# Optimization experiments

Measured on AMD Instinct MI355X. Metric: run time of the kernel, lower is better.

## Reference

```python
import jax, jax.numpy as jnp
import numpy as np

B, N, DIN = 16, 1024, 256
HEADS, OUT_DIM = 4, 256
F = OUT_DIM // HEADS  # per-head feature dim
NEG_SLOPE = 0.2
MASK_VAL = -1e9


def setup_inputs() -> dict:
    key = jax.random.key(0)
    k1, k2, k3, k4, k5, k6 = jax.random.split(key, 6)
    x = jax.random.normal(k1, (B, N, DIN), dtype=jnp.float32)
    adj = jax.random.uniform(k2, (B, N, N), dtype=jnp.float32)  # >0.5 -> edge
    # GATConv learned params (Glorot-ish scale)
    W = jax.random.normal(k3, (DIN, HEADS, F), dtype=jnp.float32) * (1.0 / np.sqrt(DIN))
    a_src = jax.random.normal(k4, (HEADS, F), dtype=jnp.float32) * (1.0 / np.sqrt(F))
    a_dst = jax.random.normal(k5, (HEADS, F), dtype=jnp.float32) * (1.0 / np.sqrt(F))
    bias = jax.random.normal(k6, (OUT_DIM,), dtype=jnp.float32) * 0.01
    return {"x": x, "adj": adj, "W": W, "a_src": a_src, "a_dst": a_dst, "bias": bias}


def reference(x, adj, W, a_src, a_dst, bias):
    # GAT over a dense adjacency mask: mathematically identical to
    # per-sample tf.where edge extraction + edge-list GATConv (softmax over
    # j with adj[b,i,j] > 0.5), but fully vectorized over the batch.
    b, n, _ = x.shape
    h = jnp.einsum('bnd,dhf->bnhf', x, W)                  # [B,N,H,F]
    e_src = jnp.einsum('bnhf,hf->bhn', h, a_src)           # source logits
    e_dst = jnp.einsum('bnhf,hf->bhn', h, a_dst)           # target logits
    # e[b,h,i,j]: edge j -> i
    e = e_dst[:, :, :, None] + e_src[:, :, None, :]        # [B,H,N,N]
    e = jax.nn.leaky_relu(e, NEG_SLOPE)
    mask = (adj > 0.5)[:, None, :, :]                      # [B,1,N,N]
    e = jnp.where(mask, e, MASK_VAL)
    attn = jax.nn.softmax(e, axis=-1)                      # softmax over sources j
    out = jnp.einsum('bhij,bjhf->bihf', attn, h)           # aggregate messages
    out = out.reshape(b, n, HEADS * F) + bias              # concat heads + bias
    return out
```

## Files before the change

### kernel.cpp

```cpp
#include <hip/hip_runtime.h>

#define B_    16
#define N_    1024
#define DIN_  256
#define H_    4
#define F_    64
#define COUT_ 256
#define NEG_  0.2f
#define LOG2E_ 1.4426950408889634f

typedef __bf16 bf16x8 __attribute__((ext_vector_type(8)));
typedef float  f32x4  __attribute__((ext_vector_type(4)));
typedef unsigned short u16x8 __attribute__((ext_vector_type(8)));
typedef unsigned short u16x4 __attribute__((ext_vector_type(4)));
typedef unsigned int   u32x4 __attribute__((ext_vector_type(4)));

__device__ __forceinline__ unsigned short f2bf(float f) {
    unsigned u = __builtin_bit_cast(unsigned, f);
    u += 0x7fffu + ((u >> 16) & 1u);
    return (unsigned short)(u >> 16);
}

__global__ __launch_bounds__(256) void prep_kernel(
    const float* __restrict__ W, unsigned short* __restrict__ Wtp) {
    const int c = blockIdx.x, k = threadIdx.x;
    const int w = c >> 6, ft = (c >> 4) & 3, l15 = c & 15;
    const int it = k >> 5, q = (k >> 3) & 3, jj = k & 7;
    const int ln = q * 16 + l15;
    Wtp[((((w * 8 + it) * 4 + ft) * 64) + ln) * 8 + jj] = f2bf(W[k * COUT_ + c]);
}

__global__ __launch_bounds__(256, 4) void stage_kernel(
    const float* __restrict__ adj, const float* __restrict__ x,
    const unsigned short* __restrict__ Wtp, const float* __restrict__ a_src,
    const float* __restrict__ a_dst, unsigned int* __restrict__ mask,
    unsigned short* __restrict__ hp, float* __restrict__ e_src,
    float* __restrict__ e_dst) {
    __shared__ unsigned short xs[16][264];
    const int w  = threadIdx.x >> 6;
    const int ln = threadIdx.x & 63;

    if (blockIdx.x < 4096) {
        const int row = blockIdx.x * 4 + w;
        const int b = row >> 10, i = row & (N_ - 1);
        const float* ar = adj + (size_t)row * N_ + ln * 4;
#pragma unroll
        for (int c = 0; c < 4; c++) {
            f32x4 v = *(const f32x4*)(ar + c * 256);
            unsigned nib = 0;
#pragma unroll
            for (int e = 0; e < 4; e++)
                nib |= (v[e] > 0.5f) ? (1u << e) : 0u;
            unsigned word = nib << ((ln & 7) * 4);
            word |= __shfl_xor(word, 1);
            word |= __shfl_xor(word, 2);
            word |= __shfl_xor(word, 4);
            if ((ln & 7) == 0) {
                const int jc = c * 8 + (ln >> 3);
                mask[(b * 32 + jc) * N_ + i] = word;
            }
        }
    } else {
        const int blk = blockIdx.x - 4096;
        const int b   = blk & 15;
        const int it0 = (blk >> 4) * 16;
        const int l15 = ln & 15;
        const int q   = ln >> 4;

#pragma unroll
        for (int s = 0; s < 4; s++) {
            const int row = w * 4 + s;
            f32x4 xv = *(const f32x4*)(x + (size_t)(b * N_ + it0 + row) * DIN_ + ln * 4);
            unsigned lo = (unsigned)f2bf(xv[0]) | ((unsigned)f2bf(xv[1]) << 16);
            unsigned hi = (unsigned)f2bf(xv[2]) | ((unsigned)f2bf(xv[3]) << 16);
            unsigned long long hb = (unsigned long long)lo | ((unsigned long long)hi << 32);
            *(unsigned long long*)&xs[row][ln * 4] = hb;
        }
        __syncthreads();

        f32x4 acc[4];
#pragma unroll
        for (int ft = 0; ft < 4; ft++) acc[ft] = (f32x4)0.0f;

        const unsigned short* wb = Wtp + (w * 8) * 4 * 64 * 8 + ln * 8;
#pragma unroll
        for (int it = 0; it < 8; it++) {
            bf16x8 af = *(const bf16x8*)&xs[l15][it * 32 + q * 8];
#pragma unroll
            for (int ft = 0; ft < 4; ft++) {
                bf16x8 bf = *((const bf16x8*)(wb + (it * 4 + ft) * 512));
                acc[ft] = __builtin_amdgcn_mfma_f32_16x16x32_bf16(af, bf, acc[ft], 0, 0, 0);
            }
        }

        const int jg = it0 >> 5;
        const int q2 = 2 * ((it0 >> 4) & 1) + (q >> 1);
#pragma unroll
        for (int ft = 0; ft < 4; ft++) {
            u16x4 hb;
#pragma unroll
            for (int r = 0; r < 4; r++) hb[r] = f2bf(acc[ft][r]);
            const size_t addr =
                (size_t)((((b * H_ + w) * 32 + jg) * 4 + ft) * 64 + q2 * 16 + l15) * 8 + (q & 1) * 4;
            *((u16x4*)(hp + addr)) = hb;
        }

        float as_v[4], ad_v[4];
#pragma unroll
        for (int ft = 0; ft < 4; ft++) {
            as_v[ft] = a_src[w * F_ + ft * 16 + l15];
            ad_v[ft] = a_dst[w * F_ + ft * 16 + l15];
        }
        float ps[4], pd[4];
#pragma unroll
        for (int r = 0; r < 4; r++) {
            ps[r] = 0.0f; pd[r] = 0.0f;
#pragma unroll
            for (int ft = 0; ft < 4; ft++) {
                ps[r] += acc[ft][r] * as_v[ft];
                pd[r] += acc[ft][r] * ad_v[ft];
            }
        }
#pragma unroll
        for (int off = 1; off <= 8; off <<= 1)
#pragma unroll
            for (int r = 0; r < 4; r++) {
                ps[r] += __shfl_xor(ps[r], off);
                pd[r] += __shfl_xor(pd[r], off);
            }
        float vs = (l15 == 0) ? ps[0] : (l15 == 1) ? ps[1] : (l15 == 2) ? ps[2] : ps[3];
        float vd = (l15 == 0) ? pd[0] : (l15 == 1) ? pd[1] : (l15 == 2) ? pd[2] : pd[3];
        if (l15 < 4) {
            const int i = it0 + q * 4 + l15;
            e_src[(b * H_ + w) * N_ + i] = vs * LOG2E_;
            e_dst[(b * H_ + w) * N_ + i] = vd * LOG2E_;
        }
    }
}

__global__ __launch_bounds__(512, 4) void gat_attn_kernel(
    const unsigned int* __restrict__ mask, const unsigned short* __restrict__ hp,
    const float* __restrict__ e_src, const float* __restrict__ e_dst,
    const float* __restrict__ bias, float* __restrict__ out) {
    const int lid = ((blockIdx.x & 7) << 6) | (blockIdx.x >> 3);
    const int b   = lid >> 5;
    const int it0 = (lid & 31) * 32;
    const int w8  = threadIdx.x >> 6;
    const int h   = w8 & 3;
    const int jh  = w8 >> 2;
    const int ln  = threadIdx.x & 63;
    const int l15 = ln & 15;
    const int q   = ln >> 4;

    __shared__ float lds[H_][2][5][64][4];

    float edv[2];
    edv[0] = e_dst[(b * H_ + h) * N_ + it0 + l15];
    edv[1] = e_dst[(b * H_ + h) * N_ + it0 + 16 + l15];

    const float* es_base          = e_src + (b * H_ + h) * N_;
    const unsigned short* hp_base = hp + (size_t)((b * H_ + h) * 32) * 2048 + ln * 8;
    const unsigned int* mk0       = mask + b * 32 * N_ + it0;

    f32x4 acc[2][4];
    f32x4 accs[2];
#pragma unroll
    for (int mt = 0; mt < 2; mt++) {
#pragma unroll
        for (int ft = 0; ft < 4; ft++) acc[mt][ft] = (f32x4)0.0f;
        accs[mt] = (f32x4)0.0f;
    }

    u16x8 ones_u;
#pragma unroll
    for (int jj = 0; jj < 8; jj++) ones_u[jj] = 0x3F80;
    const bf16x8 ones = __builtin_bit_cast(bf16x8, ones_u);

    for (int jg = jh * 16; jg < jh * 16 + 16; jg++) {
        const unsigned short* hf = hp_base + jg * 2048;
        bf16x8 bfr0 = *((const bf16x8*)(hf + 0 * 512));
        bf16x8 bfr1 = *((const bf16x8*)(hf + 1 * 512));
        bf16x8 bfr2 = *((const bf16x8*)(hf + 2 * 512));
        bf16x8 bfr3 = *((const bf16x8*)(hf + 3 * 512));
        f32x4 e0 = *(const f32x4*)(es_base + jg * 32 + q * 8);
        f32x4 e1 = *(const f32x4*)(es_base + jg * 32 + q * 8 + 4);
        const unsigned m0 = mk0[jg * N_ + l15];
        const unsigned m1 = mk0[jg * N_ + 16 + l15];

        float es8[8] = {e0[0], e0[1], e0[2], e0[3], e1[0], e1[1], e1[2], e1[3]};

        bf16x8 afr[2];
#pragma unroll
        for (int mt = 0; mt < 2; mt++) {
            const unsigned mq = ((mt ? m1 : m0) >> (q * 8)) & 0xffu;
            u32x4 up;
#pragma unroll
            for (int p2 = 0; p2 < 4; p2++) {
                float t0 = edv[mt] + es8[2 * p2];
                float t1 = edv[mt] + es8[2 * p2 + 1];
                t0 = fmaxf(t0, NEG_ * t0);
                t1 = fmaxf(t1, NEG_ * t1);
                float p0 = __builtin_amdgcn_exp2f(t0);
                float p1 = __builtin_amdgcn_exp2f(t1);
                p0 = ((mq >> (2 * p2)) & 1u) ? p0 : 0.0f;
                p1 = ((mq >> (2 * p2 + 1)) & 1u) ? p1 : 0.0f;
                up[p2] = __builtin_amdgcn_perm(__builtin_bit_cast(unsigned, p1),
                                               __builtin_bit_cast(unsigned, p0),
                                               0x07060302u);
            }
            afr[mt] = __builtin_bit_cast(bf16x8, up);
        }
#pragma unroll
        for (int mt = 0; mt < 2; mt++) {
            acc[mt][0] = __builtin_amdgcn_mfma_f32_16x16x32_bf16(afr[mt], bfr0, acc[mt][0], 0, 0, 0);
            acc[mt][1] = __builtin_amdgcn_mfma_f32_16x16x32_bf16(afr[mt], bfr1, acc[mt][1], 0, 0, 0);
            acc[mt][2] = __builtin_amdgcn_mfma_f32_16x16x32_bf16(afr[mt], bfr2, acc[mt][2], 0, 0, 0);
            acc[mt][3] = __builtin_amdgcn_mfma_f32_16x16x32_bf16(afr[mt], bfr3, acc[mt][3], 0, 0, 0);
            accs[mt]   = __builtin_amdgcn_mfma_f32_16x16x32_bf16(afr[mt], ones, accs[mt], 0, 0, 0);
        }
    }

    if (jh == 1) {
#pragma unroll
        for (int mt = 0; mt < 2; mt++) {
#pragma unroll
            for (int ft = 0; ft < 4; ft++)
                *(f32x4*)&lds[h][mt][ft][ln][0] = acc[mt][ft];
            *(f32x4*)&lds[h][mt][4][ln][0] = accs[mt];
        }
    }
    __syncthreads();
    if (jh == 0) {
#pragma unroll
        for (int mt = 0; mt < 2; mt++) {
#pragma unroll
            for (int ft = 0; ft < 4; ft++)
                acc[mt][ft] += *(const f32x4*)&lds[h][mt][ft][ln][0];
            accs[mt] += *(const f32x4*)&lds[h][mt][4][ln][0];
        }
        float bias_v[4];
#pragma unroll
        for (int ft = 0; ft < 4; ft++) bias_v[ft] = bias[h * F_ + ft * 16 + l15];
#pragma unroll
        for (int mt = 0; mt < 2; mt++) {
            f32x4 rinv;
#pragma unroll
            for (int r = 0; r < 4; r++) rinv[r] = 1.0f / accs[mt][r];
#pragma unroll
            for (int ft = 0; ft < 4; ft++)
#pragma unroll
                for (int r = 0; r < 4; r++) {
                    const int i = it0 + mt * 16 + q * 4 + r;
                    const int c = h * F_ + ft * 16 + l15;
                    out[(size_t)(b * N_ + i) * COUT_ + c] = acc[mt][ft][r] * rinv[r] + bias_v[ft];
                }
        }
    }
}

extern "C" void kernel_launch(void* const* d_in, const int* in_sizes, int n_in,
                              void* d_out, int out_size, void* d_ws, size_t ws_size,
                              hipStream_t stream) {
    const float* x     = (const float*)d_in[0];
    const float* adj   = (const float*)d_in[1];
    const float* W     = (const float*)d_in[2];
    const float* a_src = (const float*)d_in[3];
    const float* a_dst = (const float*)d_in[4];
    const float* bias  = (const float*)d_in[5];
    float* out = (float*)d_out;

    char* ws = (char*)d_ws;
    unsigned short* Wtp = (unsigned short*)ws;
    unsigned short* hp  = (unsigned short*)(ws + 131072);
    float* e_src        = (float*)(ws + 131072 + 8388608);
    float* e_dst        = (float*)(ws + 131072 + 8388608 + 262144);
    unsigned int* mask  = (unsigned int*)(ws + 131072 + 8388608 + 524288);

    prep_kernel<<<256, 256, 0, stream>>>(W, Wtp);
    stage_kernel<<<5120, 256, 0, stream>>>(adj, x, Wtp, a_src, a_dst, mask, hp, e_src, e_dst);
    gat_attn_kernel<<<512, 512, 0, stream>>>(mask, hp, e_src, e_dst, bias, out);
}
```

Baseline: 150.0 us.

## Read adjacency directly in attention kernel instead of precomputing bitmask

Drops the bit-packed mask pass from the staging kernel and has the attention kernel load the fp32 adjacency rows and threshold them inline. This avoids writing and rereading a mask buffer and shrinks the staging launch. The cost is that the attention kernel's inner loop now streams the full 64 MB adjacency, 32 bytes per row per lane, which adds memory traffic and latency on the main compute kernel's critical path.

Measured after the change: 162.6 us. 1.08x slower.

```diff
diff --git a/kernel.cpp b/kernel.cpp
--- a/kernel.cpp
+++ b/kernel.cpp
@@ -31,115 +31,92 @@
 }
 
 __global__ __launch_bounds__(256, 4) void stage_kernel(
-    const float* __restrict__ adj, const float* __restrict__ x,
-    const unsigned short* __restrict__ Wtp, const float* __restrict__ a_src,
-    const float* __restrict__ a_dst, unsigned int* __restrict__ mask,
+    const float* __restrict__ x, const unsigned short* __restrict__ Wtp,
+    const float* __restrict__ a_src, const float* __restrict__ a_dst,
     unsigned short* __restrict__ hp, float* __restrict__ e_src,
     float* __restrict__ e_dst) {
     __shared__ unsigned short xs[16][264];
     const int w  = threadIdx.x >> 6;
     const int ln = threadIdx.x & 63;
 
-    if (blockIdx.x < 4096) {
-        const int row = blockIdx.x * 4 + w;
-        const int b = row >> 10, i = row & (N_ - 1);
-        const float* ar = adj + (size_t)row * N_ + ln * 4;
-#pragma unroll
-        for (int c = 0; c < 4; c++) {
-            f32x4 v = *(const f32x4*)(ar + c * 256);
-            unsigned nib = 0;
-#pragma unroll
-            for (int e = 0; e < 4; e++)
-                nib |= (v[e] > 0.5f) ? (1u << e) : 0u;
-            unsigned word = nib << ((ln & 7) * 4);
-            word |= __shfl_xor(word, 1);
-            word |= __shfl_xor(word, 2);
-            word |= __shfl_xor(word, 4);
-            if ((ln & 7) == 0) {
-                const int jc = c * 8 + (ln >> 3);
-                mask[(b * 32 + jc) * N_ + i] = word;
-            }
-        }
-    } else {
-        const int blk = blockIdx.x - 4096;
-        const int b   = blk & 15;
-        const int it0 = (blk >> 4) * 16;
-        const int l15 = ln & 15;
-        const int q   = ln >> 4;
-
-#pragma unroll
-        for (int s = 0; s < 4; s++) {
-            const int row = w * 4 + s;
-            f32x4 xv = *(const f32x4*)(x + (size_t)(b * N_ + it0 + row) * DIN_ + ln * 4);
-            unsigned lo = (unsigned)f2bf(xv[0]) | ((unsigned)f2bf(xv[1]) << 16);
-            unsigned hi = (unsigned)f2bf(xv[2]) | ((unsigned)f2bf(xv[3]) << 16);
-            unsigned long long hb = (unsigned long long)lo | ((unsigned long long)hi << 32);
-            *(unsigned long long*)&xs[row][ln * 4] = hb;
-        }
-        __syncthreads();
-
-        f32x4 acc[4];
-#pragma unroll
-        for (int ft = 0; ft < 4; ft++) acc[ft] = (f32x4)0.0f;
-
-        const unsigned short* wb = Wtp + (w * 8) * 4 * 64 * 8 + ln * 8;
-#pragma unroll
-        for (int it = 0; it < 8; it++) {
-            bf16x8 af = *(const bf16x8*)&xs[l15][it * 32 + q * 8];
-#pragma unroll
-            for (int ft = 0; ft < 4; ft++) {
-                bf16x8 bf = *((const bf16x8*)(wb + (it * 4 + ft) * 512));
-                acc[ft] = __builtin_amdgcn_mfma_f32_16x16x32_bf16(af, bf, acc[ft], 0, 0, 0);
-            }
-        }
-
-        const int jg = it0 >> 5;
-        const int q2 = 2 * ((it0 >> 4) & 1) + (q >> 1);
+    const int blk = blockIdx.x;
+    const int b   = blk & 15;
+    const int it0 = (blk >> 4) * 16;
+    const int l15 = ln & 15;
+    const int q   = ln >> 4;
+
+#pragma unroll
+    for (int s = 0; s < 4; s++) {
+        const int row = w * 4 + s;
+        f32x4 xv = *(const f32x4*)(x + (size_t)(b * N_ + it0 + row) * DIN_ + ln * 4);
+        unsigned lo = (unsigned)f2bf(xv[0]) | ((unsigned)f2bf(xv[1]) << 16);
+        unsigned hi = (unsigned)f2bf(xv[2]) | ((unsigned)f2bf(xv[3]) << 16);
+        unsigned long long hb = (unsigned long long)lo | ((unsigned long long)hi << 32);
+        *(unsigned long long*)&xs[row][ln * 4] = hb;
+    }
+    __syncthreads();
+
+    f32x4 acc[4];
+#pragma unroll
+    for (int ft = 0; ft < 4; ft++) acc[ft] = (f32x4)0.0f;
+
+    const unsigned short* wb = Wtp + (w * 8) * 4 * 64 * 8 + ln * 8;
+#pragma unroll
+    for (int it = 0; it < 8; it++) {
+        bf16x8 af = *(const bf16x8*)&xs[l15][it * 32 + q * 8];
 #pragma unroll
         for (int ft = 0; ft < 4; ft++) {
-            u16x4 hb;
-#pragma unroll
-            for (int r = 0; r < 4; r++) hb[r] = f2bf(acc[ft][r]);
-            const size_t addr =
-                (size_t)((((b * H_ + w) * 32 + jg) * 4 + ft) * 64 + q2 * 16 + l15) * 8 + (q & 1) * 4;
-            *((u16x4*)(hp + addr)) = hb;
-        }
-
-        float as_v[4], ad_v[4];
+            bf16x8 bf = *((const bf16x8*)(wb + (it * 4 + ft) * 512));
+            acc[ft] = __builtin_amdgcn_mfma_f32_16x16x32_bf16(af, bf, acc[ft], 0, 0, 0);
+        }
+    }
+
+    const int jg = it0 >> 5;
+    const int q2 = 2 * ((it0 >> 4) & 1) + (q >> 1);
+#pragma unroll
+    for (int ft = 0; ft < 4; ft++) {
+        u16x4 hb;
+#pragma unroll
+        for (int r = 0; r < 4; r++) hb[r] = f2bf(acc[ft][r]);
+        const size_t addr =
+            (size_t)((((b * H_ + w) * 32 + jg) * 4 + ft) * 64 + q2 * 16 + l15) * 8 + (q & 1) * 4;
+        *((u16x4*)(hp + addr)) = hb;
+    }
+
+    float as_v[4], ad_v[4];
+#pragma unroll
+    for (int ft = 0; ft < 4; ft++) {
+        as_v[ft] = a_src[w * F_ + ft * 16 + l15];
+        ad_v[ft] = a_dst[w * F_ + ft * 16 + l15];
+    }
+    float ps[4], pd[4];
+#pragma unroll
+    for (int r = 0; r < 4; r++) {
+        ps[r] = 0.0f; pd[r] = 0.0f;
 #pragma unroll
         for (int ft = 0; ft < 4; ft++) {
-            as_v[ft] = a_src[w * F_ + ft * 16 + l15];
-            ad_v[ft] = a_dst[w * F_ + ft * 16 + l15];
-        }
-        float ps[4], pd[4];
+            ps[r] += acc[ft][r] * as_v[ft];
+            pd[r] += acc[ft][r] * ad_v[ft];
+        }
+    }
+#pragma unroll
+    for (int off = 1; off <= 8; off <<= 1)
 #pragma unroll
         for (int r = 0; r < 4; r++) {
-            ps[r] = 0.0f; pd[r] = 0.0f;
-#pragma unroll
-            for (int ft = 0; ft < 4; ft++) {
-                ps[r] += acc[ft][r] * as_v[ft];
-                pd[r] += acc[ft][r] * ad_v[ft];
-            }
-        }
-#pragma unroll
-        for (int off = 1; off <= 8; off <<= 1)
-#pragma unroll
-            for (int r = 0; r < 4; r++) {
-                ps[r] += __shfl_xor(ps[r], off);
-                pd[r] += __shfl_xor(pd[r], off);
-            }
-        float vs = (l15 == 0) ? ps[0] : (l15 == 1) ? ps[1] : (l15 == 2) ? ps[2] : ps[3];
-        float vd = (l15 == 0) ? pd[0] : (l15 == 1) ? pd[1] : (l15 == 2) ? pd[2] : pd[3];
-        if (l15 < 4) {
-            const int i = it0 + q * 4 + l15;
-            e_src[(b * H_ + w) * N_ + i] = vs * LOG2E_;
-            e_dst[(b * H_ + w) * N_ + i] = vd * LOG2E_;
-        }
+            ps[r] += __shfl_xor(ps[r], off);
+            pd[r] += __shfl_xor(pd[r], off);
+        }
+    float vs = (l15 == 0) ? ps[0] : (l15 == 1) ? ps[1] : (l15 == 2) ? ps[2] : ps[3];
+    float vd = (l15 == 0) ? pd[0] : (l15 == 1) ? pd[1] : (l15 == 2) ? pd[2] : pd[3];
+    if (l15 < 4) {
+        const int i = it0 + q * 4 + l15;
+        e_src[(b * H_ + w) * N_ + i] = vs * LOG2E_;
+        e_dst[(b * H_ + w) * N_ + i] = vd * LOG2E_;
     }
 }
 
 __global__ __launch_bounds__(512, 4) void gat_attn_kernel(
-    const unsigned int* __restrict__ mask, const unsigned short* __restrict__ hp,
+    const float* __restrict__ adj, const unsigned short* __restrict__ hp,
     const float* __restrict__ e_src, const float* __restrict__ e_dst,
     const float* __restrict__ bias, float* __restrict__ out) {
     const int lid = ((blockIdx.x & 7) << 6) | (blockIdx.x >> 3);
@@ -160,7 +137,8 @@
 
     const float* es_base          = e_src + (b * H_ + h) * N_;
     const unsigned short* hp_base = hp + (size_t)((b * H_ + h) * 32) * 2048 + ln * 8;
-    const unsigned int* mk0       = mask + b * 32 * N_ + it0;
+    const float* arow0 = adj + (size_t)(b * N_ + it0 + l15) * N_ + q * 8;
+    const float* arow1 = adj + (size_t)(b * N_ + it0 + 16 + l15) * N_ + q * 8;
 
     f32x4 acc[2][4];
     f32x4 accs[2];
@@ -184,15 +162,18 @@
         bf16x8 bfr3 = *((const bf16x8*)(hf + 3 * 512));
         f32x4 e0 = *(const f32x4*)(es_base + jg * 32 + q * 8);
         f32x4 e1 = *(const f32x4*)(es_base + jg * 32 + q * 8 + 4);
-        const unsigned m0 = mk0[jg * N_ + l15];
-        const unsigned m1 = mk0[jg * N_ + 16 + l15];
+        f32x4 a00 = *(const f32x4*)(arow0 + jg * 32);
+        f32x4 a01 = *(const f32x4*)(arow0 + jg * 32 + 4);
+        f32x4 a10 = *(const f32x4*)(arow1 + jg * 32);
+        f32x4 a11 = *(const f32x4*)(arow1 + jg * 32 + 4);
 
         float es8[8] = {e0[0], e0[1], e0[2], e0[3], e1[0], e1[1], e1[2], e1[3]};
+        float af8[2][8] = {{a00[0], a00[1], a00[2], a00[3], a01[0], a01[1], a01[2], a01[3]},
+                           {a10[0], a10[1], a10[2], a10[3], a11[0], a11[1], a11[2], a11[3]}};
 
         bf16x8 afr[2];
 #pragma unroll
         for (int mt = 0; mt < 2; mt++) {
-            const unsigned mq = ((mt ? m1 : m0) >> (q * 8)) & 0xffu;
             u32x4 up;
 #pragma unroll
             for (int p2 = 0; p2 < 4; p2++) {
@@ -202,8 +183,8 @@
                 t1 = fmaxf(t1, NEG_ * t1);
                 float p0 = __builtin_amdgcn_exp2f(t0);
                 float p1 = __builtin_amdgcn_exp2f(t1);
-                p0 = ((mq >> (2 * p2)) & 1u) ? p0 : 0.0f;
-                p1 = ((mq >> (2 * p2 + 1)) & 1u) ? p1 : 0.0f;
+                p0 = (af8[mt][2 * p2]     > 0.5f) ? p0 : 0.0f;
+                p1 = (af8[mt][2 * p2 + 1] > 0.5f) ? p1 : 0.0f;
                 up[p2] = __builtin_amdgcn_perm(__builtin_bit_cast(unsigned, p1),
                                                __builtin_bit_cast(unsigned, p0),
                                                0x07060302u);
@@ -274,9 +255,8 @@
     unsigned short* hp  = (unsigned short*)(ws + 131072);
     float* e_src        = (float*)(ws + 131072 + 8388608);
     float* e_dst        = (float*)(ws + 131072 + 8388608 + 262144);
-    unsigned int* mask  = (unsigned int*)(ws + 131072 + 8388608 + 524288);
 
     prep_kernel<<<256, 256, 0, stream>>>(W, Wtp);
-    stage_kernel<<<5120, 256, 0, stream>>>(adj, x, Wtp, a_src, a_dst, mask, hp, e_src, e_dst);
-    gat_attn_kernel<<<512, 512, 0, stream>>>(mask, hp, e_src, e_dst, bias, out);
-}
+    stage_kernel<<<1024, 256, 0, stream>>>(x, Wtp, a_src, a_dst, hp, e_src, e_dst);
+    gat_attn_kernel<<<512, 512, 0, stream>>>(adj, hp, e_src, e_dst, bias, out);
+}
```

## Stage e_src and mask in LDS and software-prefetch h fragments in attention loop

Applied to the files above, without the earlier changes.

Each block now loads its batch's e_src row for all heads and its 32x32 mask tile into shared memory up front, then reads them from LDS inside the loop. The j-loop is fully unrolled and double-buffers the bf16 h fragments, issuing the next iteration's global loads before the current MFMAs. This aims to hide global-load latency behind compute. It costs about 20 KB of extra LDS per block, a barrier, and more registers, which may reduce occupancy under the 512x4 launch bound.

Result: no change. 149.0 us (-0.7%).

```diff
diff --git a/kernel.cpp b/kernel.cpp
--- a/kernel.cpp
+++ b/kernel.cpp
@@ -153,14 +153,32 @@
     const int q   = ln >> 4;
 
     __shared__ float lds[H_][2][5][64][4];
+    __shared__ float es_s[H_][N_];
+    __shared__ unsigned mk_s[32][32];
+
+    {
+        const int tid = threadIdx.x;
+#pragma unroll
+        for (int p = 0; p < 2; p++) {
+            const int c  = p * 512 + tid;
+            const int h_ = c >> 8;
+            const int of = (c & 255) * 4;
+            *(f32x4*)&es_s[h_][of] =
+                *(const f32x4*)(e_src + (size_t)(b * H_ + h_) * N_ + of);
+        }
+        if (tid < 256) {
+            const int jc = tid >> 3;
+            const int i4 = (tid & 7) * 4;
+            *(u32x4*)&mk_s[jc][i4] =
+                *(const u32x4*)(mask + (size_t)(b * 32 + jc) * N_ + it0 + i4);
+        }
+    }
 
     float edv[2];
     edv[0] = e_dst[(b * H_ + h) * N_ + it0 + l15];
     edv[1] = e_dst[(b * H_ + h) * N_ + it0 + 16 + l15];
 
-    const float* es_base          = e_src + (b * H_ + h) * N_;
     const unsigned short* hp_base = hp + (size_t)((b * H_ + h) * 32) * 2048 + ln * 8;
-    const unsigned int* mk0       = mask + b * 32 * N_ + it0;
 
     f32x4 acc[2][4];
     f32x4 accs[2];
@@ -176,16 +194,30 @@
     for (int jj = 0; jj < 8; jj++) ones_u[jj] = 0x3F80;
     const bf16x8 ones = __builtin_bit_cast(bf16x8, ones_u);
 
-    for (int jg = jh * 16; jg < jh * 16 + 16; jg++) {
-        const unsigned short* hf = hp_base + jg * 2048;
-        bf16x8 bfr0 = *((const bf16x8*)(hf + 0 * 512));
-        bf16x8 bfr1 = *((const bf16x8*)(hf + 1 * 512));
-        bf16x8 bfr2 = *((const bf16x8*)(hf + 2 * 512));
-        bf16x8 bfr3 = *((const bf16x8*)(hf + 3 * 512));
-        f32x4 e0 = *(const f32x4*)(es_base + jg * 32 + q * 8);
-        f32x4 e1 = *(const f32x4*)(es_base + jg * 32 + q * 8 + 4);
-        const unsigned m0 = mk0[jg * N_ + l15];
-        const unsigned m1 = mk0[jg * N_ + 16 + l15];
+    __syncthreads();
+
+    const unsigned short* hf0 = hp_base + (size_t)(jh * 16) * 2048;
+    bf16x8 nb0 = *((const bf16x8*)(hf0 + 0 * 512));
+    bf16x8 nb1 = *((const bf16x8*)(hf0 + 1 * 512));
+    bf16x8 nb2 = *((const bf16x8*)(hf0 + 2 * 512));
+    bf16x8 nb3 = *((const bf16x8*)(hf0 + 3 * 512));
+
+#pragma unroll
+    for (int t = 0; t < 16; t++) {
+        const int jg = jh * 16 + t;
+        const bf16x8 cb0 = nb0, cb1 = nb1, cb2 = nb2, cb3 = nb3;
+        if (t < 15) {
+            const unsigned short* hfn = hp_base + (size_t)(jg + 1) * 2048;
+            nb0 = *((const bf16x8*)(hfn + 0 * 512));
+            nb1 = *((const bf16x8*)(hfn + 1 * 512));
+            nb2 = *((const bf16x8*)(hfn + 2 * 512));
+            nb3 = *((const bf16x8*)(hfn + 3 * 512));
+        }
+
+        f32x4 e0 = *(const f32x4*)&es_s[h][jg * 32 + q * 8];
+        f32x4 e1 = *(const f32x4*)&es_s[h][jg * 32 + q * 8 + 4];
+        const unsigned m0 = mk_s[jg][l15];
+        const unsigned m1 = mk_s[jg][16 + l15];
 
         float es8[8] = {e0[0], e0[1], e0[2], e0[3], e1[0], e1[1], e1[2], e1[3]};
 
@@ -212,10 +244,10 @@
         }
 #pragma unroll
         for (int mt = 0; mt < 2; mt++) {
-            acc[mt][0] = __builtin_amdgcn_mfma_f32_16x16x32_bf16(afr[mt], bfr0, acc[mt][0], 0, 0, 0);
-            acc[mt][1] = __builtin_amdgcn_mfma_f32_16x16x32_bf16(afr[mt], bfr1, acc[mt][1], 0, 0, 0);
-            acc[mt][2] = __builtin_amdgcn_mfma_f32_16x16x32_bf16(afr[mt], bfr2, acc[mt][2], 0, 0, 0);
-            acc[mt][3] = __builtin_amdgcn_mfma_f32_16x16x32_bf16(afr[mt], bfr3, acc[mt][3], 0, 0, 0);
+            acc[mt][0] = __builtin_amdgcn_mfma_f32_16x16x32_bf16(afr[mt], cb0, acc[mt][0], 0, 0, 0);
+            acc[mt][1] = __builtin_amdgcn_mfma_f32_16x16x32_bf16(afr[mt], cb1, acc[mt][1], 0, 0, 0);
+            acc[mt][2] = __builtin_amdgcn_mfma_f32_16x16x32_bf16(afr[mt], cb2, acc[mt][2], 0, 0, 0);
+            acc[mt][3] = __builtin_amdgcn_mfma_f32_16x16x32_bf16(afr[mt], cb3, acc[mt][3], 0, 0, 0);
             accs[mt]   = __builtin_amdgcn_mfma_f32_16x16x32_bf16(afr[mt], ones, accs[mt], 0, 0, 0);
         }
     }
```
